# Kernel tuning notes

Hardware: AMD Instinct MI355X
Metric: run time of the kernel (lower is better)

Reference implementation:

```python
import jax, jax.numpy as jnp
import numpy as np

EPS = 1e-5

def setup_inputs() -> dict:
    key = jax.random.key(0)
    ks = jax.random.split(key, 6)
    B, S, N, C, CZ = 1, 384, 512, 32, 128
    m_si = jax.random.normal(ks[0], (B, S, N, C), dtype=jnp.float32)
    ln_g = jnp.ones((C,), dtype=jnp.float32)
    ln_b = jnp.zeros((C,), dtype=jnp.float32)
    # torch Linear weights are (out, in)
    w_ab = jax.random.normal(ks[1], (2 * C, C), dtype=jnp.float32) / np.sqrt(C)
    w_final = jax.random.normal(ks[2], (CZ, C * C), dtype=jnp.float32) / np.sqrt(C * C)
    b_final = jax.random.normal(ks[3], (CZ,), dtype=jnp.float32) * 0.01
    return {"m_si": m_si, "ln_g": ln_g, "ln_b": ln_b, "w_ab": w_ab,
            "w_final": w_final, "b_final": b_final}

def reference(m_si, ln_g, ln_b, w_ab, w_final, b_final):
    # LayerNorm over channel dim c
    mu = jnp.mean(m_si, axis=-1, keepdims=True)
    var = jnp.mean(jnp.square(m_si - mu), axis=-1, keepdims=True)
    m = (m_si - mu) * jax.lax.rsqrt(var + EPS) * ln_g + ln_b
    # Linear (no bias) -> split into a, b : (B, s, n_seq, c)
    ab = jnp.einsum('bsnc,dc->bsnd', m, w_ab)
    c = m_si.shape[-1]
    a, b = ab[..., :c], ab[..., c:]
    n_seq = m_si.shape[-2]
    # mean over n_seq of outer products == contraction (avoids s*s*n*c*c tensor)
    o = jnp.einsum('binc,bjnd->bijcd', a, b) / n_seq  # (B, s, s, c, c)
    o = o.reshape(*o.shape[:-2], c * c)
    z = jnp.einsum('bijk,zk->bijz', o, w_final) + b_final
    return z
```

## Files before the change

kernel.cpp:

```cpp
#include <hip/hip_runtime.h>
#include <hip/hip_bf16.h>

typedef __attribute__((ext_vector_type(8))) short short8;
typedef __attribute__((ext_vector_type(4))) float f32x4;

#define S_DIM 384
#define N_DIM 512
#define C_DIM 32
#define CZ_DIM 128
#define MROWS (S_DIM * C_DIM)
#define NCELL (S_DIM * S_DIM)

__device__ __forceinline__ void async16(const void* g, void* l) {
  __builtin_amdgcn_global_load_lds(
      (const __attribute__((address_space(1))) void*)g,
      (__attribute__((address_space(3))) void*)l, 16, 0, 0);
}

__global__ __launch_bounds__(256) void prep_kernel(
    const float* __restrict__ m_si, const float* __restrict__ ln_g,
    const float* __restrict__ ln_b, const float* __restrict__ w_ab,
    __hip_bfloat16* __restrict__ Abt, __hip_bfloat16* __restrict__ Bbt) {
  const int n = blockIdx.x * 256 + threadIdx.x;
  const int s = blockIdx.y;
  const float* x = m_si + ((size_t)s * N_DIM + n) * C_DIM;

  float v[C_DIM];
#pragma unroll
  for (int i = 0; i < 8; ++i) {
    float4 t = ((const float4*)x)[i];
    v[4 * i + 0] = t.x; v[4 * i + 1] = t.y;
    v[4 * i + 2] = t.z; v[4 * i + 3] = t.w;
  }
  float sum = 0.f;
#pragma unroll
  for (int c = 0; c < C_DIM; ++c) sum += v[c];
  const float mu = sum * (1.f / 32.f);
  float sq = 0.f;
#pragma unroll
  for (int c = 0; c < C_DIM; ++c) { float d = v[c] - mu; sq += d * d; }
  const float rstd = rsqrtf(sq * (1.f / 32.f) + 1e-5f);

  float mn[C_DIM];
#pragma unroll
  for (int c = 0; c < C_DIM; ++c)
    mn[c] = (v[c] - mu) * rstd * ln_g[c] + ln_b[c];

#pragma unroll 4
  for (int d = 0; d < 32; ++d) {
    float aA = 0.f, aB = 0.f;
#pragma unroll
    for (int c = 0; c < C_DIM; ++c) {
      aA += mn[c] * w_ab[d * C_DIM + c];
      aB += mn[c] * w_ab[(d + 32) * C_DIM + c];
    }
    Abt[((size_t)(s * 32 + d)) * N_DIM + n] = __float2bfloat16(aA * (1.f / 512.f));
    Bbt[((size_t)(s * 32 + d)) * N_DIM + n] = __float2bfloat16(aB);
  }
}

__global__ __launch_bounds__(256) void conv_wf(const float* __restrict__ w_final,
                                               __hip_bfloat16* __restrict__ Wf) {
  const int i = blockIdx.x * 256 + threadIdx.x;
  Wf[i] = __float2bfloat16(w_final[i]);
}

__global__ __launch_bounds__(256, 2) void opm_main(
    const __hip_bfloat16* __restrict__ Abt, const __hip_bfloat16* __restrict__ Bbt,
    __hip_bfloat16* __restrict__ Og, int bi0) {
  __shared__ __align__(16) char smem[32768];

  const int tid = threadIdx.x;
  const int wave = tid >> 6;
  const int lane = tid & 63;
  const int fr = lane & 15;
  const int fq = lane >> 4;
  const int fqs = fq ^ ((fr >> 1) & 3);
  const int wr = wave >> 1, wc = wave & 1;

  const int f = blockIdx.y * 96 + blockIdx.x;
  const int xcd = f & 7;
  const int i_ = f >> 3;
  const int bj = xcd * 12 + (i_ % 12);
  const int biL = i_ / 12;

  const size_t m0 = (size_t)(bi0 + biL) * 128;
  const size_t n0 = (size_t)bj * 128;

  const int srow = tid >> 2;
  const int sk = (((tid & 3) ^ ((tid >> 3) & 3)) * 8);
  const __hip_bfloat16* gA = Abt + (m0 + srow) * N_DIM + sk;
  const __hip_bfloat16* gB = Bbt + (n0 + srow) * N_DIM + sk;
  const int ldst = tid * 16;

  const f32x4 fzero = {0.f, 0.f, 0.f, 0.f};
  f32x4 acc[4][4];
#pragma unroll
  for (int i = 0; i < 4; ++i)
#pragma unroll
    for (int j = 0; j < 4; ++j) acc[i][j] = fzero;

  auto stage = [&](int kt, char* base) {
    const int k0 = kt * 32;
    async16(gA + k0, base + ldst);
    async16(gA + (size_t)64 * N_DIM + k0, base + 4096 + ldst);
    async16(gB + k0, base + 8192 + ldst);
    async16(gB + (size_t)64 * N_DIM + k0, base + 12288 + ldst);
  };
  auto compute = [&](const char* base) {
    const __hip_bfloat16* As = (const __hip_bfloat16*)base;
    const __hip_bfloat16* Bs = (const __hip_bfloat16*)(base + 8192);
    short8 af[4], bfr[4];
#pragma unroll
    for (int mt = 0; mt < 4; ++mt)
      af[mt] = *(const short8*)(As + (wr * 64 + mt * 16 + fr) * 32 + fqs * 8);
#pragma unroll
    for (int nt = 0; nt < 4; ++nt)
      bfr[nt] = *(const short8*)(Bs + (wc * 64 + nt * 16 + fr) * 32 + fqs * 8);
#pragma unroll
    for (int mt = 0; mt < 4; ++mt)
#pragma unroll
      for (int nt = 0; nt < 4; ++nt)
        acc[mt][nt] = __builtin_amdgcn_mfma_f32_16x16x32_bf16(
            af[mt], bfr[nt], acc[mt][nt], 0, 0, 0);
  };

  char* buf0 = smem;
  char* buf1 = smem + 16384;
  stage(0, buf0);
  __syncthreads();
  for (int kt = 0; kt < 16; kt += 2) {
    stage(kt + 1, buf1);
    compute(buf0);
    __syncthreads();
    if (kt + 2 < 16) stage(kt + 2, buf0);
    compute(buf1);
    __syncthreads();
  }

  __hip_bfloat16* Oc = (__hip_bfloat16*)smem;
#pragma unroll
  for (int mt = 0; mt < 4; ++mt) {
#pragma unroll
    for (int nt = 0; nt < 4; ++nt) {
      const int orow_b = wr * 64 + mt * 16 + fq * 4;
      const int ocol = wc * 64 + nt * 16 + fr;
#pragma unroll
      for (int r = 0; r < 4; ++r) {
        const int orow = orow_b + r;
        const int cell = ((orow >> 5) << 2) + (ocol >> 5);
        const int kk = ((orow & 31) << 5) + (ocol & 31);
        const int sw = ((((kk >> 3) ^ (cell & 7)) << 3) | (kk & 7));
        Oc[cell * 1024 + sw] = __float2bfloat16(acc[mt][nt][r]);
      }
    }
  }
  __syncthreads();

  const __hip_bfloat16* OcR = (const __hip_bfloat16*)smem;
#pragma unroll
  for (int j = 0; j < 8; ++j) {
    const int lc = j * 256 + tid;
    const int cellL = lc >> 7;
    const int ch = lc & 127;
    const int phys = (ch & ~7) | ((ch & 7) ^ (cellL & 7));
    const short8 val = *(const short8*)(OcR + cellL * 1024 + phys * 8);
    const int li = cellL >> 2, lj = cellL & 3;
    __hip_bfloat16* dst =
        Og + ((size_t)((biL * 4 + li) * S_DIM + (bj * 4 + lj))) * 1024 + ch * 8;
    *(short8*)dst = val;
  }
}

__global__ __launch_bounds__(256, 2) void zgemm(
    const __hip_bfloat16* __restrict__ Og, const __hip_bfloat16* __restrict__ Wf,
    const float* __restrict__ b_final, float* __restrict__ out) {
  __shared__ __align__(16) char smem[32768];

  const int tid = threadIdx.x;
  const int wave = tid >> 6;
  const int lane = tid & 63;
  const int fr = lane & 15;
  const int fq = lane >> 4;
  const int fqs = fq ^ ((fr >> 1) & 3);
  const int wr = wave >> 1, wc = wave & 1;
  const size_t cell0 = (size_t)blockIdx.x * 128;

  const int srow = tid >> 2;
  const int sk = (((tid & 3) ^ ((tid >> 3) & 3)) * 8);
  const __hip_bfloat16* gO = Og + (cell0 + srow) * 1024 + sk;
  const __hip_bfloat16* gW = Wf + (size_t)srow * 1024 + sk;
  const int ldst = tid * 16;

  const f32x4 fzero = {0.f, 0.f, 0.f, 0.f};
  f32x4 acc[4][4];
#pragma unroll
  for (int i = 0; i < 4; ++i)
#pragma unroll
    for (int j = 0; j < 4; ++j) acc[i][j] = fzero;

  auto stage = [&](int kt, char* base) {
    const int k0 = kt * 32;
    async16(gO + k0, base + ldst);
    async16(gO + (size_t)64 * 1024 + k0, base + 4096 + ldst);
    async16(gW + k0, base + 8192 + ldst);
    async16(gW + (size_t)64 * 1024 + k0, base + 12288 + ldst);
  };
  auto compute = [&](const char* base) {
    const __hip_bfloat16* As = (const __hip_bfloat16*)base;
    const __hip_bfloat16* Bs = (const __hip_bfloat16*)(base + 8192);
    short8 af[4], bfr[4];
#pragma unroll
    for (int mt = 0; mt < 4; ++mt)
      af[mt] = *(const short8*)(As + (wr * 64 + mt * 16 + fr) * 32 + fqs * 8);
#pragma unroll
    for (int nt = 0; nt < 4; ++nt)
      bfr[nt] = *(const short8*)(Bs + (wc * 64 + nt * 16 + fr) * 32 + fqs * 8);
#pragma unroll
    for (int mt = 0; mt < 4; ++mt)
#pragma unroll
      for (int nt = 0; nt < 4; ++nt)
        acc[mt][nt] = __builtin_amdgcn_mfma_f32_16x16x32_bf16(
            af[mt], bfr[nt], acc[mt][nt], 0, 0, 0);
  };

  char* buf0 = smem;
  char* buf1 = smem + 16384;
  stage(0, buf0);
  __syncthreads();
  for (int kt = 0; kt < 32; kt += 2) {
    stage(kt + 1, buf1);
    compute(buf0);
    __syncthreads();
    if (kt + 2 < 32) stage(kt + 2, buf0);
    compute(buf1);
    __syncthreads();
  }

#pragma unroll
  for (int nt = 0; nt < 4; ++nt) {
    const int zcol = wc * 64 + nt * 16 + fr;
    const float bz = b_final[zcol];
#pragma unroll
    for (int mt = 0; mt < 4; ++mt) {
      const size_t zrow = cell0 + wr * 64 + mt * 16 + fq * 4;
#pragma unroll
      for (int r = 0; r < 4; ++r)
        out[(zrow + r) * CZ_DIM + zcol] = acc[mt][nt][r] + bz;
    }
  }
}

__global__ __launch_bounds__(256, 2) void fused_opm(
    const __hip_bfloat16* __restrict__ Abt, const __hip_bfloat16* __restrict__ Bbt,
    const __hip_bfloat16* __restrict__ Wf, const float* __restrict__ b_final,
    float* __restrict__ out) {
  __shared__ __align__(16) char smem[32768];
  const int tid = threadIdx.x;
  const int wave = tid >> 6;
  const int lane = tid & 63;
  const int fr = lane & 15;
  const int fq = lane >> 4;
  const int fqs = fq ^ ((fr >> 1) & 3);
  const int wr = wave >> 1, wc = wave & 1;
  const int bi = blockIdx.y, bj = blockIdx.x;
  const size_t m0 = (size_t)bi * 128;
  const size_t n0 = (size_t)bj * 128;
  const int srow = tid >> 2;
  const int sk = (((tid & 3) ^ ((tid >> 3) & 3)) * 8);
  const __hip_bfloat16* gA = Abt + (m0 + srow) * N_DIM + sk;
  const __hip_bfloat16* gB = Bbt + (n0 + srow) * N_DIM + sk;
  const int ldst = tid * 16;

  const f32x4 fzero = {0.f, 0.f, 0.f, 0.f};
  f32x4 acc[4][4];
#pragma unroll
  for (int i = 0; i < 4; ++i)
#pragma unroll
    for (int j = 0; j < 4; ++j) acc[i][j] = fzero;

  auto stage = [&](int kt, char* base) {
    const int k0 = kt * 32;
    async16(gA + k0, base + ldst);
    async16(gA + (size_t)64 * N_DIM + k0, base + 4096 + ldst);
    async16(gB + k0, base + 8192 + ldst);
    async16(gB + (size_t)64 * N_DIM + k0, base + 12288 + ldst);
  };
  auto compute = [&](const char* base) {
    const __hip_bfloat16* As = (const __hip_bfloat16*)base;
    const __hip_bfloat16* Bs = (const __hip_bfloat16*)(base + 8192);
    short8 af[4], bfr[4];
#pragma unroll
    for (int mt = 0; mt < 4; ++mt)
      af[mt] = *(const short8*)(As + (wr * 64 + mt * 16 + fr) * 32 + fqs * 8);
#pragma unroll
    for (int nt = 0; nt < 4; ++nt)
      bfr[nt] = *(const short8*)(Bs + (wc * 64 + nt * 16 + fr) * 32 + fqs * 8);
#pragma unroll
    for (int mt = 0; mt < 4; ++mt)
#pragma unroll
      for (int nt = 0; nt < 4; ++nt)
        acc[mt][nt] = __builtin_amdgcn_mfma_f32_16x16x32_bf16(
            af[mt], bfr[nt], acc[mt][nt], 0, 0, 0);
  };

  char* buf0 = smem;
  char* buf1 = smem + 16384;
  stage(0, buf0);
  __syncthreads();
  for (int kt = 0; kt < 16; kt += 2) {
    stage(kt + 1, buf1);
    compute(buf0);
    __syncthreads();
    if (kt + 2 < 16) stage(kt + 2, buf0);
    compute(buf1);
    __syncthreads();
  }

  __hip_bfloat16* Oc = (__hip_bfloat16*)smem;
#pragma unroll
  for (int mt = 0; mt < 4; ++mt) {
#pragma unroll
    for (int nt = 0; nt < 4; ++nt) {
      const int orow_b = wr * 64 + mt * 16 + fq * 4;
      const int ocol = wc * 64 + nt * 16 + fr;
#pragma unroll
      for (int r = 0; r < 4; ++r) {
        const int orow = orow_b + r;
        const int cell = ((orow >> 5) << 2) + (ocol >> 5);
        const int kk = ((orow & 31) << 5) + (ocol & 31);
        const int sw = ((((kk >> 3) ^ (cell & 7)) << 3) | (kk & 7));
        Oc[cell * 1024 + sw] = __float2bfloat16(acc[mt][nt][r]);
      }
    }
  }
  __syncthreads();

  f32x4 zacc0 = fzero, zacc1 = fzero;
  const int zt0 = wave * 2;
  const int xr = fr & 7;
  for (int kk = 0; kk < 32; ++kk) {
    const int slot = kk * 4 + fq;
    const short8 oa = *(const short8*)(Oc + fr * 1024 + ((slot ^ xr) << 3));
    const short8 wb0 =
        *(const short8*)(Wf + (size_t)((zt0 + 0) * 16 + fr) * 1024 + kk * 32 + fq * 8);
    const short8 wb1 =
        *(const short8*)(Wf + (size_t)((zt0 + 1) * 16 + fr) * 1024 + kk * 32 + fq * 8);
    zacc0 = __builtin_amdgcn_mfma_f32_16x16x32_bf16(oa, wb0, zacc0, 0, 0, 0);
    zacc1 = __builtin_amdgcn_mfma_f32_16x16x32_bf16(oa, wb1, zacc1, 0, 0, 0);
  }

  const int i0 = bi * 4, j0 = bj * 4;
#pragma unroll
  for (int t = 0; t < 2; ++t) {
    const int zcol = (zt0 + t) * 16 + fr;
    const float bz = b_final[zcol];
    const f32x4 za = t ? zacc1 : zacc0;
#pragma unroll
    for (int r = 0; r < 4; ++r) {
      const int cell = fq * 4 + r;
      const int li = cell >> 2, lj = cell & 3;
      out[((size_t)(i0 + li) * S_DIM + (j0 + lj)) * CZ_DIM + zcol] = za[r] + bz;
    }
  }
}

extern "C" void kernel_launch(void* const* d_in, const int* in_sizes, int n_in,
                              void* d_out, int out_size, void* d_ws, size_t ws_size,
                              hipStream_t stream) {
  const float* m_si = (const float*)d_in[0];
  const float* ln_g = (const float*)d_in[1];
  const float* ln_b = (const float*)d_in[2];
  const float* w_ab = (const float*)d_in[3];
  const float* w_final = (const float*)d_in[4];
  const float* b_final = (const float*)d_in[5];
  float* out = (float*)d_out;

  char* ws = (char*)d_ws;
  __hip_bfloat16* Abt = (__hip_bfloat16*)ws;
  __hip_bfloat16* Bbt = (__hip_bfloat16*)(ws + (size_t)MROWS * N_DIM * 2);
  __hip_bfloat16* Wf = (__hip_bfloat16*)(ws + (size_t)MROWS * N_DIM * 4);
  const size_t base = (size_t)MROWS * N_DIM * 4 + 262144;
  __hip_bfloat16* Og = (__hip_bfloat16*)(ws + base);

  prep_kernel<<<dim3(2, S_DIM), 256, 0, stream>>>(m_si, ln_g, ln_b, w_ab, Abt, Bbt);
  conv_wf<<<dim3((CZ_DIM * 1024) / 256), 256, 0, stream>>>(w_final, Wf);

  static const int cands[] = {2, 3, 4, 6, 8, 12, 16, 24, 32};
  int nslab = 0;
  for (int c : cands) {
    if (base + ((size_t)NCELL / c) * 1024 * 2 <= ws_size) { nslab = c; break; }
  }

  if (nslab) {
    const int biPer = 96 / nslab;
    const int cellsPer = NCELL / nslab;
    for (int s = 0; s < nslab; ++s) {
      opm_main<<<dim3(96, biPer), 256, 0, stream>>>(Abt, Bbt, Og, s * biPer);
      zgemm<<<dim3(cellsPer / 128), 256, 0, stream>>>(
          Og, Wf, b_final, out + (size_t)s * cellsPer * CZ_DIM);
    }
  } else {
    fused_opm<<<dim3(96, 96), 256, 0, stream>>>(Abt, Bbt, Wf, b_final, out);
  }
}
```

Before: 367.4 us.

## Merge OPM and z-GEMM into one kernel with double-buffered slabs for overlap

Combines the outer-product GEMM and the final z-projection GEMM into a single kernel. Blocks are split by index, so each launch runs the z-GEMM for the previous slab alongside the outer-product GEMM for the current slab. Two ping-pong intermediate buffers let the two stages overlap inside one grid, and the tail of each launch is shared across the stages. This cuts the launch count and filling the GPU between dependent launches, at the cost of twice the workspace and a branchier kernel with more register pressure.

```diff
diff --git a/kernel.cpp b/kernel.cpp
--- a/kernel.cpp
+++ b/kernel.cpp
@@ -65,9 +65,11 @@
   Wf[i] = __float2bfloat16(w_final[i]);
 }
 
-__global__ __launch_bounds__(256, 2) void opm_main(
+__global__ __launch_bounds__(256, 2) void combined(
     const __hip_bfloat16* __restrict__ Abt, const __hip_bfloat16* __restrict__ Bbt,
-    __hip_bfloat16* __restrict__ Og, int bi0) {
+    const __hip_bfloat16* __restrict__ Wf, const float* __restrict__ b_final,
+    __hip_bfloat16* __restrict__ OgW, const __hip_bfloat16* __restrict__ OgR,
+    float* __restrict__ outp, int bi0, int zN) {
   __shared__ __align__(16) char smem[32768];
 
   const int tid = threadIdx.x;
@@ -77,176 +79,159 @@
   const int fq = lane >> 4;
   const int fqs = fq ^ ((fr >> 1) & 3);
   const int wr = wave >> 1, wc = wave & 1;
-
-  const int f = blockIdx.y * 96 + blockIdx.x;
-  const int xcd = f & 7;
-  const int i_ = f >> 3;
-  const int bj = xcd * 12 + (i_ % 12);
-  const int biL = i_ / 12;
-
-  const size_t m0 = (size_t)(bi0 + biL) * 128;
-  const size_t n0 = (size_t)bj * 128;
-
   const int srow = tid >> 2;
   const int sk = (((tid & 3) ^ ((tid >> 3) & 3)) * 8);
-  const __hip_bfloat16* gA = Abt + (m0 + srow) * N_DIM + sk;
-  const __hip_bfloat16* gB = Bbt + (n0 + srow) * N_DIM + sk;
   const int ldst = tid * 16;
-
   const f32x4 fzero = {0.f, 0.f, 0.f, 0.f};
-  f32x4 acc[4][4];
-#pragma unroll
-  for (int i = 0; i < 4; ++i)
-#pragma unroll
-    for (int j = 0; j < 4; ++j) acc[i][j] = fzero;
-
-  auto stage = [&](int kt, char* base) {
-    const int k0 = kt * 32;
-    async16(gA + k0, base + ldst);
-    async16(gA + (size_t)64 * N_DIM + k0, base + 4096 + ldst);
-    async16(gB + k0, base + 8192 + ldst);
-    async16(gB + (size_t)64 * N_DIM + k0, base + 12288 + ldst);
-  };
-  auto compute = [&](const char* base) {
-    const __hip_bfloat16* As = (const __hip_bfloat16*)base;
-    const __hip_bfloat16* Bs = (const __hip_bfloat16*)(base + 8192);
-    short8 af[4], bfr[4];
-#pragma unroll
-    for (int mt = 0; mt < 4; ++mt)
-      af[mt] = *(const short8*)(As + (wr * 64 + mt * 16 + fr) * 32 + fqs * 8);
-#pragma unroll
-    for (int nt = 0; nt < 4; ++nt)
-      bfr[nt] = *(const short8*)(Bs + (wc * 64 + nt * 16 + fr) * 32 + fqs * 8);
-#pragma unroll
-    for (int mt = 0; mt < 4; ++mt)
+
+  if (blockIdx.x < (unsigned)zN) {
+    const size_t cell0 = (size_t)blockIdx.x * 128;
+    const __hip_bfloat16* gO = OgR + (cell0 + srow) * 1024 + sk;
+    const __hip_bfloat16* gW = Wf + (size_t)srow * 1024 + sk;
+
+    f32x4 acc[4][4];
+#pragma unroll
+    for (int i = 0; i < 4; ++i)
+#pragma unroll
+      for (int j = 0; j < 4; ++j) acc[i][j] = fzero;
+
+    auto stage = [&](int kt, char* base) {
+      const int k0 = kt * 32;
+      async16(gO + k0, base + ldst);
+      async16(gO + (size_t)64 * 1024 + k0, base + 4096 + ldst);
+      async16(gW + k0, base + 8192 + ldst);
+      async16(gW + (size_t)64 * 1024 + k0, base + 12288 + ldst);
+    };
+    auto compute = [&](const char* base) {
+      const __hip_bfloat16* As = (const __hip_bfloat16*)base;
+      const __hip_bfloat16* Bs = (const __hip_bfloat16*)(base + 8192);
+      short8 af[4], bfr[4];
+#pragma unroll
+      for (int mt = 0; mt < 4; ++mt)
+        af[mt] = *(const short8*)(As + (wr * 64 + mt * 16 + fr) * 32 + fqs * 8);
 #pragma unroll
       for (int nt = 0; nt < 4; ++nt)
-        acc[mt][nt] = __builtin_amdgcn_mfma_f32_16x16x32_bf16(
-            af[mt], bfr[nt], acc[mt][nt], 0, 0, 0);
-  };
-
-  char* buf0 = smem;
-  char* buf1 = smem + 16384;
-  stage(0, buf0);
-  __syncthreads();
-  for (int kt = 0; kt < 16; kt += 2) {
-    stage(kt + 1, buf1);
-    compute(buf0);
+        bfr[nt] = *(const short8*)(Bs + (wc * 64 + nt * 16 + fr) * 32 + fqs * 8);
+#pragma unroll
+      for (int mt = 0; mt < 4; ++mt)
+#pragma unroll
+        for (int nt = 0; nt < 4; ++nt)
+          acc[mt][nt] = __builtin_amdgcn_mfma_f32_16x16x32_bf16(
+              af[mt], bfr[nt], acc[mt][nt], 0, 0, 0);
+    };
+
+    char* buf0 = smem;
+    char* buf1 = smem + 16384;
+    stage(0, buf0);
     __syncthreads();
-    if (kt + 2 < 16) stage(kt + 2, buf0);
-    compute(buf1);
+    for (int kt = 0; kt < 32; kt += 2) {
+      stage(kt + 1, buf1);
+      compute(buf0);
+      __syncthreads();
+      if (kt + 2 < 32) stage(kt + 2, buf0);
+      compute(buf1);
+      __syncthreads();
+    }
+
+#pragma unroll
+    for (int nt = 0; nt < 4; ++nt) {
+      const int zcol = wc * 64 + nt * 16 + fr;
+      const float bz = b_final[zcol];
+#pragma unroll
+      for (int mt = 0; mt < 4; ++mt) {
+        const size_t zrow = cell0 + wr * 64 + mt * 16 + fq * 4;
+#pragma unroll
+        for (int r = 0; r < 4; ++r)
+          outp[(zrow + r) * CZ_DIM + zcol] = acc[mt][nt][r] + bz;
+      }
+    }
+  } else {
+    const int f = blockIdx.x - zN;
+    const int xcd = f & 7;
+    const int i_ = f >> 3;
+    const int bj = xcd * 12 + (i_ % 12);
+    const int biL = i_ / 12;
+
+    const size_t m0 = (size_t)(bi0 + biL) * 128;
+    const size_t n0 = (size_t)bj * 128;
+    const __hip_bfloat16* gA = Abt + (m0 + srow) * N_DIM + sk;
+    const __hip_bfloat16* gB = Bbt + (n0 + srow) * N_DIM + sk;
+
+    f32x4 acc[4][4];
+#pragma unroll
+    for (int i = 0; i < 4; ++i)
+#pragma unroll
+      for (int j = 0; j < 4; ++j) acc[i][j] = fzero;
+
+    auto stage = [&](int kt, char* base) {
+      const int k0 = kt * 32;
+      async16(gA + k0, base + ldst);
+      async16(gA + (size_t)64 * N_DIM + k0, base + 4096 + ldst);
+      async16(gB + k0, base + 8192 + ldst);
+      async16(gB + (size_t)64 * N_DIM + k0, base + 12288 + ldst);
+    };
+    auto compute = [&](const char* base) {
+      const __hip_bfloat16* As = (const __hip_bfloat16*)base;
+      const __hip_bfloat16* Bs = (const __hip_bfloat16*)(base + 8192);
+      short8 af[4], bfr[4];
+#pragma unroll
+      for (int mt = 0; mt < 4; ++mt)
+        af[mt] = *(const short8*)(As + (wr * 64 + mt * 16 + fr) * 32 + fqs * 8);
+#pragma unroll
+      for (int nt = 0; nt < 4; ++nt)
+        bfr[nt] = *(const short8*)(Bs + (wc * 64 + nt * 16 + fr) * 32 + fqs * 8);
+#pragma unroll
+      for (int mt = 0; mt < 4; ++mt)
+#pragma unroll
+        for (int nt = 0; nt < 4; ++nt)
+          acc[mt][nt] = __builtin_amdgcn_mfma_f32_16x16x32_bf16(
+              af[mt], bfr[nt], acc[mt][nt], 0, 0, 0);
+    };
+
+    char* buf0 = smem;
+    char* buf1 = smem + 16384;
+    stage(0, buf0);
     __syncthreads();
-  }
-
-  __hip_bfloat16* Oc = (__hip_bfloat16*)smem;
-#pragma unroll
-  for (int mt = 0; mt < 4; ++mt) {
-#pragma unroll
-    for (int nt = 0; nt < 4; ++nt) {
-      const int orow_b = wr * 64 + mt * 16 + fq * 4;
-      const int ocol = wc * 64 + nt * 16 + fr;
-#pragma unroll
-      for (int r = 0; r < 4; ++r) {
-        const int orow = orow_b + r;
-        const int cell = ((orow >> 5) << 2) + (ocol >> 5);
-        const int kk = ((orow & 31) << 5) + (ocol & 31);
-        const int sw = ((((kk >> 3) ^ (cell & 7)) << 3) | (kk & 7));
-        Oc[cell * 1024 + sw] = __float2bfloat16(acc[mt][nt][r]);
+    for (int kt = 0; kt < 16; kt += 2) {
+      stage(kt + 1, buf1);
+      compute(buf0);
+      __syncthreads();
+      if (kt + 2 < 16) stage(kt + 2, buf0);
+      compute(buf1);
+      __syncthreads();
+    }
+
+    __hip_bfloat16* Oc = (__hip_bfloat16*)smem;
+#pragma unroll
+    for (int mt = 0; mt < 4; ++mt) {
+#pragma unroll
+      for (int nt = 0; nt < 4; ++nt) {
+        const int orow_b = wr * 64 + mt * 16 + fq * 4;
+        const int ocol = wc * 64 + nt * 16 + fr;
+#pragma unroll
+        for (int r = 0; r < 4; ++r) {
+          const int orow = orow_b + r;
+          const int cell = ((orow >> 5) << 2) + (ocol >> 5);
+          const int kk = ((orow & 31) << 5) + (ocol & 31);
+          const int sw = ((((kk >> 3) ^ (cell & 7)) << 3) | (kk & 7));
+          Oc[cell * 1024 + sw] = __float2bfloat16(acc[mt][nt][r]);
+        }
       }
     }
-  }
-  __syncthreads();
-
-  const __hip_bfloat16* OcR = (const __hip_bfloat16*)smem;
-#pragma unroll
-  for (int j = 0; j < 8; ++j) {
-    const int lc = j * 256 + tid;
-    const int cellL = lc >> 7;
-    const int ch = lc & 127;
-    const int phys = (ch & ~7) | ((ch & 7) ^ (cellL & 7));
-    const short8 val = *(const short8*)(OcR + cellL * 1024 + phys * 8);
-    const int li = cellL >> 2, lj = cellL & 3;
-    __hip_bfloat16* dst =
-        Og + ((size_t)((biL * 4 + li) * S_DIM + (bj * 4 + lj))) * 1024 + ch * 8;
-    *(short8*)dst = val;
-  }
-}
-
-__global__ __launch_bounds__(256, 2) void zgemm(
-    const __hip_bfloat16* __restrict__ Og, const __hip_bfloat16* __restrict__ Wf,
-    const float* __restrict__ b_final, float* __restrict__ out) {
-  __shared__ __align__(16) char smem[32768];
-
-  const int tid = threadIdx.x;
-  const int wave = tid >> 6;
-  const int lane = tid & 63;
-  const int fr = lane & 15;
-  const int fq = lane >> 4;
-  const int fqs = fq ^ ((fr >> 1) & 3);
-  const int wr = wave >> 1, wc = wave & 1;
-  const size_t cell0 = (size_t)blockIdx.x * 128;
-
-  const int srow = tid >> 2;
-  const int sk = (((tid & 3) ^ ((tid >> 3) & 3)) * 8);
-  const __hip_bfloat16* gO = Og + (cell0 + srow) * 1024 + sk;
-  const __hip_bfloat16* gW = Wf + (size_t)srow * 1024 + sk;
-  const int ldst = tid * 16;
-
-  const f32x4 fzero = {0.f, 0.f, 0.f, 0.f};
-  f32x4 acc[4][4];
-#pragma unroll
-  for (int i = 0; i < 4; ++i)
-#pragma unroll
-    for (int j = 0; j < 4; ++j) acc[i][j] = fzero;
-
-  auto stage = [&](int kt, char* base) {
-    const int k0 = kt * 32;
-    async16(gO + k0, base + ldst);
-    async16(gO + (size_t)64 * 1024 + k0, base + 4096 + ldst);
-    async16(gW + k0, base + 8192 + ldst);
-    async16(gW + (size_t)64 * 1024 + k0, base + 12288 + ldst);
-  };
-  auto compute = [&](const char* base) {
-    const __hip_bfloat16* As = (const __hip_bfloat16*)base;
-    const __hip_bfloat16* Bs = (const __hip_bfloat16*)(base + 8192);
-    short8 af[4], bfr[4];
-#pragma unroll
-    for (int mt = 0; mt < 4; ++mt)
-      af[mt] = *(const short8*)(As + (wr * 64 + mt * 16 + fr) * 32 + fqs * 8);
-#pragma unroll
-    for (int nt = 0; nt < 4; ++nt)
-      bfr[nt] = *(const short8*)(Bs + (wc * 64 + nt * 16 + fr) * 32 + fqs * 8);
-#pragma unroll
-    for (int mt = 0; mt < 4; ++mt)
-#pragma unroll
-      for (int nt = 0; nt < 4; ++nt)
-        acc[mt][nt] = __builtin_amdgcn_mfma_f32_16x16x32_bf16(
-            af[mt], bfr[nt], acc[mt][nt], 0, 0, 0);
-  };
-
-  char* buf0 = smem;
-  char* buf1 = smem + 16384;
-  stage(0, buf0);
-  __syncthreads();
-  for (int kt = 0; kt < 32; kt += 2) {
-    stage(kt + 1, buf1);
-    compute(buf0);
     __syncthreads();
-    if (kt + 2 < 32) stage(kt + 2, buf0);
-    compute(buf1);
-    __syncthreads();
-  }
-
-#pragma unroll
-  for (int nt = 0; nt < 4; ++nt) {
-    const int zcol = wc * 64 + nt * 16 + fr;
-    const float bz = b_final[zcol];
-#pragma unroll
-    for (int mt = 0; mt < 4; ++mt) {
-      const size_t zrow = cell0 + wr * 64 + mt * 16 + fq * 4;
-#pragma unroll
-      for (int r = 0; r < 4; ++r)
-        out[(zrow + r) * CZ_DIM + zcol] = acc[mt][nt][r] + bz;
+
+    const __hip_bfloat16* OcR = (const __hip_bfloat16*)smem;
+#pragma unroll
+    for (int j = 0; j < 8; ++j) {
+      const int lc = j * 256 + tid;
+      const int cellL = lc >> 7;
+      const int ch = lc & 127;
+      const int phys = (ch & ~7) | ((ch & 7) ^ (cellL & 7));
+      const short8 val = *(const short8*)(OcR + cellL * 1024 + phys * 8);
+      const int li = cellL >> 2, lj = cellL & 3;
+      __hip_bfloat16* dst =
+          OgW + ((size_t)((biL * 4 + li) * S_DIM + (bj * 4 + lj))) * 1024 + ch * 8;
+      *(short8*)dst = val;
     }
   }
 }
@@ -381,10 +366,35 @@
   __hip_bfloat16* Bbt = (__hip_bfloat16*)(ws + (size_t)MROWS * N_DIM * 2);
   __hip_bfloat16* Wf = (__hip_bfloat16*)(ws + (size_t)MROWS * N_DIM * 4);
   const size_t base = (size_t)MROWS * N_DIM * 4 + 262144;
-  __hip_bfloat16* Og = (__hip_bfloat16*)(ws + base);
 
   prep_kernel<<<dim3(2, S_DIM), 256, 0, stream>>>(m_si, ln_g, ln_b, w_ab, Abt, Bbt);
   conv_wf<<<dim3((CZ_DIM * 1024) / 256), 256, 0, stream>>>(w_final, Wf);
+
+  static const int pairs[] = {4, 8, 16};
+  int npair = 0;
+  for (int c : pairs) {
+    if (base + 2 * ((size_t)NCELL / c) * 1024 * 2 <= ws_size) { npair = c; break; }
+  }
+
+  if (npair) {
+    const int biPer = 96 / npair;
+    const size_t cellsPer = (size_t)NCELL / npair;
+    const size_t slabBytes = cellsPer * 1024 * 2;
+    const int zB = (int)(cellsPer / 128);
+    const int oB = 96 * biPer;
+    __hip_bfloat16* Ob[2] = {(__hip_bfloat16*)(ws + base),
+                             (__hip_bfloat16*)(ws + base + slabBytes)};
+    for (int s = 0; s <= npair; ++s) {
+      const int zN = (s > 0) ? zB : 0;
+      const int grid = zN + ((s < npair) ? oB : 0);
+      combined<<<grid, 256, 0, stream>>>(
+          Abt, Bbt, Wf, b_final,
+          Ob[s & 1], Ob[(s + 1) & 1],
+          out + (size_t)(s - 1) * cellsPer * CZ_DIM,
+          s * biPer, zN);
+    }
+    return;
+  }
 
   static const int cands[] = {2, 3, 4, 6, 8, 12, 16, 24, 32};
   int nslab = 0;
@@ -394,11 +404,16 @@
 
   if (nslab) {
     const int biPer = 96 / nslab;
-    const int cellsPer = NCELL / nslab;
+    const size_t cellsPer = (size_t)NCELL / nslab;
+    const int zB = (int)(cellsPer / 128);
+    const int oB = 96 * biPer;
+    __hip_bfloat16* Og = (__hip_bfloat16*)(ws + base);
     for (int s = 0; s < nslab; ++s) {
-      opm_main<<<dim3(96, biPer), 256, 0, stream>>>(Abt, Bbt, Og, s * biPer);
-      zgemm<<<dim3(cellsPer / 128), 256, 0, stream>>>(
-          Og, Wf, b_final, out + (size_t)s * cellsPer * CZ_DIM);
+      combined<<<oB, 256, 0, stream>>>(Abt, Bbt, Wf, b_final, Og, Og,
+                                       out, s * biPer, 0);
+      combined<<<zB, 256, 0, stream>>>(Abt, Bbt, Wf, b_final, Og, Og,
+                                       out + (size_t)s * cellsPer * CZ_DIM,
+                                       0, zB);
     }
   } else {
     fused_opm<<<dim3(96, 96), 256, 0, stream>>>(Abt, Bbt, Wf, b_final, out);
```

Result: slower. 391.7 us (+6.6%).
